# Kernel tuning notes

Measured on AMD Instinct MI355X. Metric: run time of the kernel, lower is better.

## Reference

```python
import jax, jax.numpy as jnp
import numpy as np

# module config (matches init_kwargs, single stream, groups=1)
N, I = 4, 64            # batch, input channels
CR, CA, CO = 64, 64, 64 # recurrent, attention, out channels
HEADS, S = 4, 3         # heads, spatial kernel
HC = CA // HEADS        # head channels = 16
H, W = 48, 48
INIT_I, INIT_F = -1.0, 1.0


def _conv(x, w, padding):
    # x: [N,C,H,W], w: [O,C,kh,kw]
    return jax.lax.conv_general_dilated(
        x, w, window_strides=(1, 1), padding=padding,
        dimension_numbers=('NCHW', 'OIHW', 'NCHW'))


def setup_inputs() -> dict:
    key = jax.random.key(0)
    ks = jax.random.split(key, 8)
    std = 0.05
    x = jax.random.normal(ks[0], (N, I, H, W), jnp.float32)
    W_in = jax.random.normal(ks[1], (CR, I), jnp.float32) * std      # 1x1 input conv
    b_in = jnp.zeros((CR,), jnp.float32)
    # 4 combos (xx, xh, hx, hh), each a 3x3 conv CR->CA, no bias
    Wq = jax.random.normal(ks[2], (4, CA, CR, S, S), jnp.float32) * std * (HC ** -0.5)
    Wk = jax.random.normal(ks[3], (4, CA, CR, S, S), jnp.float32) * std
    Wv = jax.random.normal(ks[4], (4, CA, CR, S, S), jnp.float32) * std
    # gate projections: 4 gates (i,f,g,o) x 4 attn branches, each 1x1 CA->CR
    Wproj = jax.random.normal(ks[5], (4, 4, CR, CA), jnp.float32) * std * 0.5
    b_gates = jnp.array([INIT_I, INIT_F, 0.0, 0.0], jnp.float32)[:, None] * jnp.ones((4, CR), jnp.float32)
    W_out = jax.random.normal(ks[6], (CO, CR), jnp.float32) * std    # 1x1 out conv
    b_out = jnp.zeros((CO,), jnp.float32)
    return {"x": x, "W_in": W_in, "b_in": b_in, "Wq": Wq, "Wk": Wk, "Wv": Wv,
            "Wproj": Wproj, "b_gates": b_gates, "W_out": W_out, "b_out": b_out}


def reference(x, W_in, b_in, Wq, Wk, Wv, Wproj, b_gates, W_out, b_out):
    n, _, hh, ww = x.shape
    # input projection (Accumulate of one 1x1 conv, bias 0)
    xin = jnp.einsum('nchw,oc->nohw', x, W_in) + b_in[None, :, None, None]
    h = jnp.zeros_like(xin)  # cold start: past is empty -> h = c = 0
    pairs = ((xin, xin), (xin, h), (h, xin), (h, h))
    attns = []
    for idx, (query, token) in enumerate(pairs):
        # q: SAME-padded 3x3 conv -> Q = H*W tokens; k/v: VALID -> D = (H-2)*(W-2)
        q = _conv(query, Wq[idx], 'SAME').reshape(n, HEADS, HC, -1)    # [n,h,c,Q]
        k = _conv(token, Wk[idx], 'VALID').reshape(n, HEADS, HC, -1)   # [n,h,c,D]
        v = _conv(token, Wv[idx], 'VALID').reshape(n, HEADS, HC, -1)   # [n,h,c,D]
        w = jax.nn.softmax(jnp.einsum('nhcq,nhcd->nhqd', q, k), axis=-1)
        a = jnp.einsum('nhcd,nhqd->nhcq', v, w).reshape(n, CA, hh, ww)
        attns.append(a)
    A = jnp.stack(attns, axis=0)  # [4, n, CA, H, W]
    # Accumulate of 4 1x1 projections per gate + gate bias
    pre = jnp.einsum('anchw,gaoc->gnohw', A, Wproj) + b_gates[:, None, :, None, None]
    i = jax.nn.sigmoid(pre[0])
    f = jax.nn.sigmoid(pre[1])
    g = jnp.tanh(pre[2])
    o = jax.nn.sigmoid(pre[3])
    c = i * g          # c_prev = 0, so f*c_prev vanishes
    hout = o * jnp.tanh(c)  # dropout p=0 -> identity
    return jnp.einsum('nchw,oc->nohw', hout, W_out) + b_out[None, :, None, None]
```

## Files before the change

### kernel.cpp

```cpp
#include <hip/hip_runtime.h>
#include <math.h>

#define NB   4
#define CIN  64
#define HH   48
#define WW   48
#define HW   2304
#define DH   46
#define DW   46
#define DD   2116
#define NHEAD 4
#define HC   16
#define NT   136
#define QTL  144

typedef short  s4 __attribute__((ext_vector_type(4)));
typedef short  s8 __attribute__((ext_vector_type(8)));
typedef float  f4 __attribute__((ext_vector_type(4)));

__global__ __launch_bounds__(256) void k_xin(const float* __restrict__ x,
                                             const float* __restrict__ Win,
                                             const float* __restrict__ bin,
                                             unsigned short* __restrict__ xb) {
    int cell = blockIdx.x * 256 + threadIdx.x;
    if (cell >= 2500) return;
    int n = blockIdx.y, ocg = blockIdx.z;
    int cy = cell / 50, cx = cell - cy * 50;
    float a[4] = {0.f, 0.f, 0.f, 0.f};
    if (cy >= 1 && cy <= 48 && cx >= 1 && cx <= 48) {
        int px = (cy - 1) * 48 + (cx - 1);
        const float* xp = x + (size_t)(n * CIN) * HW + px;
        #pragma unroll
        for (int j = 0; j < 4; ++j) a[j] = bin[ocg * 4 + j];
        #pragma unroll 8
        for (int ic = 0; ic < CIN; ++ic) {
            float xv = xp[ic * HW];
            a[0] += Win[(ocg * 4 + 0) * CIN + ic] * xv;
            a[1] += Win[(ocg * 4 + 1) * CIN + ic] * xv;
            a[2] += Win[(ocg * 4 + 2) * CIN + ic] * xv;
            a[3] += Win[(ocg * 4 + 3) * CIN + ic] * xv;
        }
    }
    s8 st;
    #pragma unroll
    for (int j = 0; j < 4; ++j) {
        unsigned u = __builtin_bit_cast(unsigned, a[j]);
        st[j] = (short)(u >> 16);
        float lo = a[j] - __builtin_bit_cast(float, u & 0xffff0000u);
        st[4 + j] = (short)(__builtin_bit_cast(unsigned, lo) >> 16);
    }
    *(s8*)(xb + ((size_t)(n * 2500 + cell)) * 128 + ocg * 8) = st;
}

__global__ __launch_bounds__(256) void k_wcvt(const float* __restrict__ Wq,
                                              const float* __restrict__ Wk,
                                              const float* __restrict__ Wv,
                                              unsigned short* __restrict__ Wb) {
    int bx = blockIdx.x;
    int cq = bx / 9, tap = bx - cq * 9;
    int cv = cq >> 2, ocq = cq & 3;
    const float* src = (cv == 0) ? Wq : (cv == 1) ? Wk : (cv == 2) ? Wv
                                                      : (Wv + 2 * CIN * CIN * 9);
    int t = threadIdx.x;
    int m = t >> 4, kl = t & 15, quad = kl >> 2, j = kl & 3;
    #pragma unroll
    for (int kq = 0; kq < 4; ++kq) {
        float v = src[((size_t)(ocq * 16 + m) * CIN + kq * 16 + kl) * 9 + tap];
        unsigned u = __builtin_bit_cast(unsigned, v);
        float lo = v - __builtin_bit_cast(float, u & 0xffff0000u);
        size_t base = ((size_t)(cq * 9 + tap) * 4 + kq) * 512 + m * 32 + quad * 8 + j;
        Wb[base]     = (unsigned short)(u >> 16);
        Wb[base + 4] = (unsigned short)(__builtin_bit_cast(unsigned, lo) >> 16);
    }
}

__global__ __launch_bounds__(256, 3) void k_conv(const unsigned short* __restrict__ xb,
                                                 const unsigned short* __restrict__ Wb,
                                                 float* __restrict__ q0, float* __restrict__ k0,
                                                 float* __restrict__ v0, float* __restrict__ v2) {
    int y = blockIdx.x, n = blockIdx.y, cv = blockIdx.z;
    float* ob; int outw, pd;
    if (cv == 0)      { ob = q0; outw = 48; pd = 0; }
    else if (cv == 1) { ob = k0; outw = 46; pd = 1; }
    else if (cv == 2) { ob = v0; outw = 46; pd = 1; }
    else              { ob = v2; outw = 46; pd = 1; }
    if (y >= outw) return;
    int lane = threadIdx.x & 63, wv = threadIdx.x >> 6;
    int m16 = lane & 15, quad = lane >> 4;
    const unsigned short* Wt = Wb + (size_t)(cv * 4 + wv) * 9 * 2048 + m16 * 32 + quad * 8;
    const unsigned short* B0 = xb + ((size_t)n * 2500 + (size_t)(y + pd) * 50 + pd + m16) * 128 + quad * 8;

    f4 a0 = {0.f, 0.f, 0.f, 0.f}, a1 = a0, a2 = a0;

    s8 w[4], c0[4], c1[4], c2[4];
    #pragma unroll
    for (int kq = 0; kq < 4; ++kq) {
        w[kq]  = *(const s8*)(Wt + kq * 512);
        c0[kq] = *(const s8*)(B0 + kq * 32);
        c1[kq] = *(const s8*)(B0 + 16 * 128 + kq * 32);
        c2[kq] = *(const s8*)(B0 + 32 * 128 + kq * 32);
    }

    #pragma unroll
    for (int tap = 0; tap < 9; ++tap) {
        s8 wn[4], n0[4], n1[4], n2[4];
        if (tap < 8) {
            int tn = tap + 1;
            int dy = tn / 3, dx = tn - dy * 3;
            const unsigned short* bp = B0 + (size_t)(dy * 50 + dx) * 128;
            const unsigned short* wp = Wt + tn * 2048;
            #pragma unroll
            for (int kq = 0; kq < 4; ++kq) {
                wn[kq] = *(const s8*)(wp + kq * 512);
                n0[kq] = *(const s8*)(bp + kq * 32);
                n1[kq] = *(const s8*)(bp + 16 * 128 + kq * 32);
                n2[kq] = *(const s8*)(bp + 32 * 128 + kq * 32);
            }
        }
        #pragma unroll
        for (int kq = 0; kq < 4; ++kq) {
            s4 ah  = __builtin_shufflevector(w[kq], w[kq], 0, 1, 2, 3);
            s4 al  = __builtin_shufflevector(w[kq], w[kq], 4, 5, 6, 7);
            s4 bh0 = __builtin_shufflevector(c0[kq], c0[kq], 0, 1, 2, 3);
            s4 bl0 = __builtin_shufflevector(c0[kq], c0[kq], 4, 5, 6, 7);
            s4 bh1 = __builtin_shufflevector(c1[kq], c1[kq], 0, 1, 2, 3);
            s4 bl1 = __builtin_shufflevector(c1[kq], c1[kq], 4, 5, 6, 7);
            s4 bh2 = __builtin_shufflevector(c2[kq], c2[kq], 0, 1, 2, 3);
            s4 bl2 = __builtin_shufflevector(c2[kq], c2[kq], 4, 5, 6, 7);
            a0 = __builtin_amdgcn_mfma_f32_16x16x16bf16_1k(ah, bh0, a0, 0, 0, 0);
            a1 = __builtin_amdgcn_mfma_f32_16x16x16bf16_1k(ah, bh1, a1, 0, 0, 0);
            a2 = __builtin_amdgcn_mfma_f32_16x16x16bf16_1k(ah, bh2, a2, 0, 0, 0);
            a0 = __builtin_amdgcn_mfma_f32_16x16x16bf16_1k(al, bh0, a0, 0, 0, 0);
            a1 = __builtin_amdgcn_mfma_f32_16x16x16bf16_1k(al, bh1, a1, 0, 0, 0);
            a2 = __builtin_amdgcn_mfma_f32_16x16x16bf16_1k(al, bh2, a2, 0, 0, 0);
            a0 = __builtin_amdgcn_mfma_f32_16x16x16bf16_1k(ah, bl0, a0, 0, 0, 0);
            a1 = __builtin_amdgcn_mfma_f32_16x16x16bf16_1k(ah, bl1, a1, 0, 0, 0);
            a2 = __builtin_amdgcn_mfma_f32_16x16x16bf16_1k(ah, bl2, a2, 0, 0, 0);
        }
        if (tap < 8) {
            #pragma unroll
            for (int kq = 0; kq < 4; ++kq) {
                w[kq] = wn[kq]; c0[kq] = n0[kq]; c1[kq] = n1[kq]; c2[kq] = n2[kq];
            }
        }
    }

    size_t outsz = (size_t)outw * outw;
    float* opb = ob + (size_t)(n * CIN + wv * 16 + quad * 4) * outsz + (size_t)y * outw;
    {
        float* op = opb + m16;
        op[0] = a0.x; op[outsz] = a0.y; op[2 * outsz] = a0.z; op[3 * outsz] = a0.w;
        op = opb + 16 + m16;
        op[0] = a1.x; op[outsz] = a1.y; op[2 * outsz] = a1.z; op[3 * outsz] = a1.w;
    }
    if (32 + m16 < outw) {
        float* op = opb + 32 + m16;
        op[0] = a2.x; op[outsz] = a2.y; op[2 * outsz] = a2.z; op[3 * outsz] = a2.w;
    }
}

__global__ __launch_bounds__(256) void k_cvt(const float* __restrict__ q0,
                                             const float* __restrict__ k0,
                                             const float* __restrict__ v0,
                                             unsigned short* __restrict__ Qb,
                                             unsigned short* __restrict__ Kb,
                                             unsigned short* __restrict__ Vb) {
    __shared__ float sm[272];
    int bx = blockIdx.x, nh = blockIdx.y;
    int n = nh >> 2, h = nh & 3;
    int t = threadIdx.x;
    {
        int c = t >> 4, q = t & 15;
        float val = q0[(size_t)(n * CIN + h * HC + c) * HW + bx * 16 + q];
        sm[c * 17 + q] = val;
        __syncthreads();
        int q2 = t >> 4, c2 = t & 15;
        float v = sm[c2 * 17 + q2];
        unsigned u = __builtin_bit_cast(unsigned, v);
        unsigned short* dst = Qb + (size_t)(nh * QTL + bx) * 512;
        dst[t] = (unsigned short)(u >> 16);
        float lo = v - __builtin_bit_cast(float, u & 0xffff0000u);
        dst[256 + t] = (unsigned short)(__builtin_bit_cast(unsigned, lo) >> 16);
    }
    if (bx < NT) {
        __syncthreads();
        int c = t >> 4, d = t & 15;
        int dgl = bx * 16 + d;
        float kv = (dgl < DD) ? k0[(size_t)(n * CIN + h * HC + c) * DD + dgl] : 0.f;
        sm[c * 17 + d] = kv;
        __syncthreads();
        {
            int d2 = t >> 4, c2 = t & 15;
            float v = sm[c2 * 17 + d2];
            unsigned u = __builtin_bit_cast(unsigned, v);
            unsigned short* dst = Kb + (size_t)(nh * NT + bx) * 512;
            dst[t] = (unsigned short)(u >> 16);
            float lo = v - __builtin_bit_cast(float, u & 0xffff0000u);
            dst[256 + t] = (unsigned short)(__builtin_bit_cast(unsigned, lo) >> 16);
        }
        {
            float vv = (dgl < DD) ? v0[(size_t)(n * CIN + h * HC + c) * DD + dgl] : 0.f;
            unsigned u = __builtin_bit_cast(unsigned, vv);
            unsigned short* dst = Vb + (size_t)(nh * NT + bx) * 512;
            dst[t] = (unsigned short)(u >> 16);
            float lo = vv - __builtin_bit_cast(float, u & 0xffff0000u);
            dst[256 + t] = (unsigned short)(__builtin_bit_cast(unsigned, lo) >> 16);
        }
    }
}

__global__ __launch_bounds__(256) void k_mattn(const unsigned short* __restrict__ Qb,
                                               const unsigned short* __restrict__ Kb,
                                               const unsigned short* __restrict__ Vb,
                                               float* __restrict__ part) {
    __shared__ float sO[4][4][256];
    __shared__ float sl[4][4][64];
    int strip = blockIdx.x >> 1, hb = blockIdx.x & 1, nh = blockIdx.y;
    int lane = threadIdx.x & 63, wv = threadIdx.x >> 6;
    int ds = hb * 4 + wv;
    int q16 = lane & 15, quad = lane >> 4;
    int foff = q16 * 16 + quad * 4;

    s4 qh[4], ql[4];
    #pragma unroll
    for (int j = 0; j < 4; ++j) {
        const unsigned short* Qp = Qb + (size_t)(nh * QTL + strip * 4 + j) * 512 + foff;
        qh[j] = *(const s4*)(Qp);
        ql[j] = *(const s4*)(Qp + 256);
    }
    f4 O[4];
    float l[4];
    #pragma unroll
    for (int j = 0; j < 4; ++j) { O[j] = (f4){0.f, 0.f, 0.f, 0.f}; l[j] = 0.f; }

    const unsigned short* Kp = Kb + (size_t)(nh * NT + ds * 17) * 512 + foff;
    const unsigned short* Vp = Vb + (size_t)(nh * NT + ds * 17) * 512 + foff;
    s4 khi = *(const s4*)(Kp);
    s4 klo = *(const s4*)(Kp + 256);
    s4 vhi = *(const s4*)(Vp);
    s4 vlo = *(const s4*)(Vp + 256);

    for (int it = 0; it < 17; ++it) {
        int nxt = (it < 16) ? (it + 1) * 512 : 0;
        s4 nkhi = *(const s4*)(Kp + nxt);
        s4 nklo = *(const s4*)(Kp + nxt + 256);
        s4 nvhi = *(const s4*)(Vp + nxt);
        s4 nvlo = *(const s4*)(Vp + nxt + 256);

        #pragma unroll
        for (int j = 0; j < 4; ++j) {
            f4 c1 = (f4){0.f, 0.f, 0.f, 0.f};
            c1 = __builtin_amdgcn_mfma_f32_16x16x16bf16_1k(khi, qh[j], c1, 0, 0, 0);
            c1 = __builtin_amdgcn_mfma_f32_16x16x16bf16_1k(klo, qh[j], c1, 0, 0, 0);
            c1 = __builtin_amdgcn_mfma_f32_16x16x16bf16_1k(khi, ql[j], c1, 0, 0, 0);
            float p0 = __expf(c1.x), p1 = __expf(c1.y);
            float p2 = __expf(c1.z), p3 = __expf(c1.w);
            l[j] += (p0 + p1) + (p2 + p3);
            unsigned u0 = __builtin_bit_cast(unsigned, p0);
            unsigned u1 = __builtin_bit_cast(unsigned, p1);
            unsigned u2 = __builtin_bit_cast(unsigned, p2);
            unsigned u3 = __builtin_bit_cast(unsigned, p3);
            s4 ph;
            ph.x = (short)(u0 >> 16); ph.y = (short)(u1 >> 16);
            ph.z = (short)(u2 >> 16); ph.w = (short)(u3 >> 16);
            float r0 = p0 - __builtin_bit_cast(float, u0 & 0xffff0000u);
            float r1 = p1 - __builtin_bit_cast(float, u1 & 0xffff0000u);
            float r2 = p2 - __builtin_bit_cast(float, u2 & 0xffff0000u);
            float r3 = p3 - __builtin_bit_cast(float, u3 & 0xffff0000u);
            s4 pl;
            pl.x = (short)(__builtin_bit_cast(unsigned, r0) >> 16);
            pl.y = (short)(__builtin_bit_cast(unsigned, r1) >> 16);
            pl.z = (short)(__builtin_bit_cast(unsigned, r2) >> 16);
            pl.w = (short)(__builtin_bit_cast(unsigned, r3) >> 16);
            O[j] = __builtin_amdgcn_mfma_f32_16x16x16bf16_1k(vhi, ph, O[j], 0, 0, 0);
            O[j] = __builtin_amdgcn_mfma_f32_16x16x16bf16_1k(vlo, ph, O[j], 0, 0, 0);
            O[j] = __builtin_amdgcn_mfma_f32_16x16x16bf16_1k(vhi, pl, O[j], 0, 0, 0);
        }
        khi = nkhi; klo = nklo; vhi = nvhi; vlo = nvlo;
    }

    #pragma unroll
    for (int j = 0; j < 4; ++j) {
        sO[wv][j][(quad * 4 + 0) * 16 + q16] = O[j].x;
        sO[wv][j][(quad * 4 + 1) * 16 + q16] = O[j].y;
        sO[wv][j][(quad * 4 + 2) * 16 + q16] = O[j].z;
        sO[wv][j][(quad * 4 + 3) * 16 + q16] = O[j].w;
        sl[wv][j][quad * 16 + q16] = l[j];
    }
    __syncthreads();
    int t = threadIdx.x;
    float* pb = part + (size_t)((nh * 36 + strip) * 2 + hb) * 1280;
    #pragma unroll
    for (int j = 0; j < 4; ++j)
        pb[j * 256 + t] = (sO[0][j][t] + sO[1][j][t]) + (sO[2][j][t] + sO[3][j][t]);
    {
        int j2 = t >> 6, i2 = t & 63;
        pb[1024 + t] = (sl[0][j2][i2] + sl[1][j2][i2]) + (sl[2][j2][i2] + sl[3][j2][i2]);
    }
}

__global__ __launch_bounds__(256) void k_acomb(const float* __restrict__ part,
                                               float* __restrict__ a0) {
    int strip = blockIdx.x, nh = blockIdx.y;
    int n = nh >> 2, h = nh & 3;
    const float* b0 = part + (size_t)((nh * 36 + strip) * 2) * 1280;
    const float* b1 = b0 + 1280;
    int t = threadIdx.x;
    int q = t & 15, c = t >> 4;
    #pragma unroll
    for (int j = 0; j < 4; ++j) {
        float lsum = 0.f;
        #pragma unroll
        for (int qd = 0; qd < 4; ++qd)
            lsum += b0[1024 + j * 64 + qd * 16 + q] + b1[1024 + j * 64 + qd * 16 + q];
        float inv = 1.f / (lsum - 60.f);
        float v = (b0[j * 256 + c * 16 + q] + b1[j * 256 + c * 16 + q]) * inv;
        a0[(size_t)(n * CIN + h * HC + c) * HW + strip * 64 + j * 16 + q] = v;
    }
}

__global__ __launch_bounds__(256) void k_mean(const float* __restrict__ v2,
                                              float* __restrict__ a2m) {
    int n = blockIdx.x >> 6, c = blockIdx.x & 63;
    const float* p = v2 + (size_t)(n * CIN + c) * DD;
    float s = 0.f;
    for (int d = threadIdx.x; d < DD; d += 256) s += p[d];
    #pragma unroll
    for (int off = 32; off > 0; off >>= 1) s += __shfl_down(s, off);
    __shared__ float red[4];
    int lane = threadIdx.x & 63, wv = threadIdx.x >> 6;
    if (lane == 0) red[wv] = s;
    __syncthreads();
    if (threadIdx.x == 0)
        a2m[blockIdx.x] = (red[0] + red[1] + red[2] + red[3]) * (1.f / 2116.f);
}

__global__ __launch_bounds__(256) void k_const2(const float* __restrict__ Wproj,
                                                const float* __restrict__ bg,
                                                const float* __restrict__ a2m,
                                                float* __restrict__ c2) {
    int n = blockIdx.x;
    int t = threadIdx.x;
    if (t >= 192) return;
    int gi = t >> 6, o = t & 63;
    int g = (gi == 0) ? 0 : (gi == 1) ? 2 : 3;
    float acc = bg[g * CIN + o];
    const float* wp = Wproj + ((size_t)(g * 4 + 2) * CIN + o) * CIN;
    for (int c = 0; c < CIN; ++c) acc += wp[c] * a2m[n * CIN + c];
    c2[(gi * NB + n) * CIN + o] = acc;
}

__global__ __launch_bounds__(256) void k_gates(const float* __restrict__ a0,
                                               const float* __restrict__ c2,
                                               const float* __restrict__ Wproj,
                                               const float* __restrict__ Wout,
                                               const float* __restrict__ bout,
                                               float* __restrict__ out) {
    __shared__ float a0s[64][16];
    __shared__ float wps[3][64][64];
    __shared__ float hs[16][68];
    int n = blockIdx.y;
    int p0 = blockIdx.x * 16;
    int tid = threadIdx.x;

    for (int idx = tid; idx < 1024; idx += 256) {
        int c = idx >> 4, px = idx & 15;
        a0s[c][px] = a0[(size_t)(n * CIN + c) * HW + p0 + px];
    }
    for (int idx = tid; idx < 12288; idx += 256) {
        int o = idx & 63; int rest = idx >> 6; int c = rest & 63; int gi = rest >> 6;
        int g = (gi == 0) ? 0 : (gi == 1) ? 2 : 3;
        wps[gi][c][o] = Wproj[((size_t)(g * 4 + 0) * CIN + o) * CIN + c];
    }
    __syncthreads();

    int o = tid & 63, pg = tid >> 6;
    float pi[4], pgt[4], po[4];
    {
        float ci = c2[(0 * NB + n) * CIN + o];
        float cg = c2[(1 * NB + n) * CIN + o];
        float co = c2[(2 * NB + n) * CIN + o];
        #pragma unroll
        for (int j = 0; j < 4; ++j) { pi[j] = ci; pgt[j] = cg; po[j] = co; }
    }
    const float4* a4 = (const float4*)&a0s[0][0];
    #pragma unroll 4
    for (int c = 0; c < 64; ++c) {
        float4 av = a4[c * 4 + pg];
        float w0 = wps[0][c][o], w1 = wps[1][c][o], w2 = wps[2][c][o];
        pi[0]  += w0 * av.x; pi[1]  += w0 * av.y; pi[2]  += w0 * av.z; pi[3]  += w0 * av.w;
        pgt[0] += w1 * av.x; pgt[1] += w1 * av.y; pgt[2] += w1 * av.z; pgt[3] += w1 * av.w;
        po[0]  += w2 * av.x; po[1]  += w2 * av.y; po[2]  += w2 * av.z; po[3]  += w2 * av.w;
    }
    #pragma unroll
    for (int j = 0; j < 4; ++j) {
        float ii = 1.f / (1.f + __expf(-pi[j]));
        float gg = tanhf(pgt[j]);
        float oo = 1.f / (1.f + __expf(-po[j]));
        float cc = ii * gg;
        hs[pg * 4 + j][o] = oo * tanhf(cc);
    }
    __syncthreads();
    float acc[4];
    float bo = bout[o];
    #pragma unroll
    for (int j = 0; j < 4; ++j) acc[j] = bo;
    const float* wo = Wout + o * CIN;
    #pragma unroll 2
    for (int cg_ = 0; cg_ < 16; ++cg_) {
        float w0 = wo[cg_ * 4 + 0], w1 = wo[cg_ * 4 + 1], w2 = wo[cg_ * 4 + 2], w3 = wo[cg_ * 4 + 3];
        #pragma unroll
        for (int j = 0; j < 4; ++j) {
            const float4 hv = *(const float4*)&hs[pg * 4 + j][cg_ * 4];
            acc[j] += w0 * hv.x + w1 * hv.y + w2 * hv.z + w3 * hv.w;
        }
    }
    #pragma unroll
    for (int j = 0; j < 4; ++j)
        out[(size_t)(n * CIN + o) * HW + p0 + pg * 4 + j] = acc[j];
}

extern "C" void kernel_launch(void* const* d_in, const int* in_sizes, int n_in,
                              void* d_out, int out_size, void* d_ws, size_t ws_size,
                              hipStream_t stream) {
    const float* x     = (const float*)d_in[0];
    const float* W_in  = (const float*)d_in[1];
    const float* b_in  = (const float*)d_in[2];
    const float* Wq    = (const float*)d_in[3];
    const float* Wk    = (const float*)d_in[4];
    const float* Wv    = (const float*)d_in[5];
    const float* Wproj = (const float*)d_in[6];
    const float* b_g   = (const float*)d_in[7];
    const float* W_out = (const float*)d_in[8];
    const float* b_out = (const float*)d_in[9];
    float* out = (float*)d_out;

    float* q0   = (float*)d_ws;
    float* k0   = q0 + 589824;
    float* v0   = k0 + 541696;
    float* v2   = v0 + 541696;
    float* a0   = v2 + 541696;
    float* a2m  = a0 + 589824;
    float* c2   = a2m + 256;
    float* part = c2 + 768;
    unsigned short* Qb = (unsigned short*)(part + 1474560);
    unsigned short* Kb = Qb + (size_t)16 * QTL * 512;
    unsigned short* Vb = Kb + (size_t)16 * NT * 512;
    unsigned short* xb = Vb + (size_t)16 * NT * 512;
    unsigned short* Wb = xb + (size_t)4 * 2500 * 128;

    k_xin   <<<dim3(10, 4, 16), 256, 0, stream>>>(x, W_in, b_in, xb);
    k_wcvt  <<<dim3(144), 256, 0, stream>>>(Wq, Wk, Wv, Wb);
    k_conv  <<<dim3(48, 4, 4), 256, 0, stream>>>(xb, Wb, q0, k0, v0, v2);
    k_cvt   <<<dim3(144, 16), 256, 0, stream>>>(q0, k0, v0, Qb, Kb, Vb);
    k_mattn <<<dim3(72, 16), 256, 0, stream>>>(Qb, Kb, Vb, part);
    k_acomb <<<dim3(36, 16), 256, 0, stream>>>(part, a0);
    k_mean  <<<dim3(256), 256, 0, stream>>>(v2, a2m);
    k_const2<<<dim3(4), 256, 0, stream>>>(Wproj, b_g, a2m, c2);
    k_gates <<<dim3(144, 4), 256, 0, stream>>>(a0, c2, Wproj, W_out, b_out, out);
}
```

Before: 206.9 us.

## Merge prep kernels, fold attention combine and gate constants into gates kernel

Combines the input-projection and weight-conversion kernels into one launch with block-index dispatch. Removes the k_acomb and k_const2 kernels by computing the softmax normalisation and branch-2 gate constants inside k_gates directly from the partial attention buffers. Also adds sched_group_barrier hints in the conv MFMA loop to interleave loads and MFMAs. This cuts launches and the a0 round trip through global memory, at the cost of redundant per-block constant computation in k_gates.

```diff
diff --git a/kernel.cpp b/kernel.cpp
--- a/kernel.cpp
+++ b/kernel.cpp
@@ -18,59 +18,61 @@
 typedef short  s8 __attribute__((ext_vector_type(8)));
 typedef float  f4 __attribute__((ext_vector_type(4)));
 
-__global__ __launch_bounds__(256) void k_xin(const float* __restrict__ x,
-                                             const float* __restrict__ Win,
-                                             const float* __restrict__ bin,
-                                             unsigned short* __restrict__ xb) {
-    int cell = blockIdx.x * 256 + threadIdx.x;
-    if (cell >= 2500) return;
-    int n = blockIdx.y, ocg = blockIdx.z;
-    int cy = cell / 50, cx = cell - cy * 50;
-    float a[4] = {0.f, 0.f, 0.f, 0.f};
-    if (cy >= 1 && cy <= 48 && cx >= 1 && cx <= 48) {
-        int px = (cy - 1) * 48 + (cx - 1);
-        const float* xp = x + (size_t)(n * CIN) * HW + px;
-        #pragma unroll
-        for (int j = 0; j < 4; ++j) a[j] = bin[ocg * 4 + j];
-        #pragma unroll 8
-        for (int ic = 0; ic < CIN; ++ic) {
-            float xv = xp[ic * HW];
-            a[0] += Win[(ocg * 4 + 0) * CIN + ic] * xv;
-            a[1] += Win[(ocg * 4 + 1) * CIN + ic] * xv;
-            a[2] += Win[(ocg * 4 + 2) * CIN + ic] * xv;
-            a[3] += Win[(ocg * 4 + 3) * CIN + ic] * xv;
-        }
-    }
-    s8 st;
-    #pragma unroll
-    for (int j = 0; j < 4; ++j) {
-        unsigned u = __builtin_bit_cast(unsigned, a[j]);
-        st[j] = (short)(u >> 16);
-        float lo = a[j] - __builtin_bit_cast(float, u & 0xffff0000u);
-        st[4 + j] = (short)(__builtin_bit_cast(unsigned, lo) >> 16);
-    }
-    *(s8*)(xb + ((size_t)(n * 2500 + cell)) * 128 + ocg * 8) = st;
-}
-
-__global__ __launch_bounds__(256) void k_wcvt(const float* __restrict__ Wq,
-                                              const float* __restrict__ Wk,
-                                              const float* __restrict__ Wv,
-                                              unsigned short* __restrict__ Wb) {
-    int bx = blockIdx.x;
-    int cq = bx / 9, tap = bx - cq * 9;
-    int cv = cq >> 2, ocq = cq & 3;
-    const float* src = (cv == 0) ? Wq : (cv == 1) ? Wk : (cv == 2) ? Wv
-                                                      : (Wv + 2 * CIN * CIN * 9);
-    int t = threadIdx.x;
-    int m = t >> 4, kl = t & 15, quad = kl >> 2, j = kl & 3;
-    #pragma unroll
-    for (int kq = 0; kq < 4; ++kq) {
-        float v = src[((size_t)(ocq * 16 + m) * CIN + kq * 16 + kl) * 9 + tap];
-        unsigned u = __builtin_bit_cast(unsigned, v);
-        float lo = v - __builtin_bit_cast(float, u & 0xffff0000u);
-        size_t base = ((size_t)(cq * 9 + tap) * 4 + kq) * 512 + m * 32 + quad * 8 + j;
-        Wb[base]     = (unsigned short)(u >> 16);
-        Wb[base + 4] = (unsigned short)(__builtin_bit_cast(unsigned, lo) >> 16);
+__global__ __launch_bounds__(256) void k_xw(const float* __restrict__ x,
+                                            const float* __restrict__ Win,
+                                            const float* __restrict__ bin,
+                                            const float* __restrict__ Wq,
+                                            const float* __restrict__ Wk,
+                                            const float* __restrict__ Wv,
+                                            unsigned short* __restrict__ xb,
+                                            unsigned short* __restrict__ Wb) {
+    int b = blockIdx.x;
+    if (b < 640) {
+        int bx = b % 10, n = (b / 10) & 3, ocg = b / 40;
+        int cell = bx * 256 + threadIdx.x;
+        if (cell >= 2500) return;
+        int cy = cell / 50, cx = cell - cy * 50;
+        float a[4] = {0.f, 0.f, 0.f, 0.f};
+        if (cy >= 1 && cy <= 48 && cx >= 1 && cx <= 48) {
+            int px = (cy - 1) * 48 + (cx - 1);
+            const float* xp = x + (size_t)(n * CIN) * HW + px;
+            #pragma unroll
+            for (int j = 0; j < 4; ++j) a[j] = bin[ocg * 4 + j];
+            #pragma unroll 8
+            for (int ic = 0; ic < CIN; ++ic) {
+                float xv = xp[ic * HW];
+                a[0] += Win[(ocg * 4 + 0) * CIN + ic] * xv;
+                a[1] += Win[(ocg * 4 + 1) * CIN + ic] * xv;
+                a[2] += Win[(ocg * 4 + 2) * CIN + ic] * xv;
+                a[3] += Win[(ocg * 4 + 3) * CIN + ic] * xv;
+            }
+        }
+        s8 st;
+        #pragma unroll
+        for (int j = 0; j < 4; ++j) {
+            unsigned u = __builtin_bit_cast(unsigned, a[j]);
+            st[j] = (short)(u >> 16);
+            float lo = a[j] - __builtin_bit_cast(float, u & 0xffff0000u);
+            st[4 + j] = (short)(__builtin_bit_cast(unsigned, lo) >> 16);
+        }
+        *(s8*)(xb + ((size_t)(n * 2500 + cell)) * 128 + ocg * 8) = st;
+    } else {
+        int bx = b - 640;
+        int cq = bx / 9, tap = bx - cq * 9;
+        int cv = cq >> 2, ocq = cq & 3;
+        const float* src = (cv == 0) ? Wq : (cv == 1) ? Wk : (cv == 2) ? Wv
+                                                          : (Wv + 2 * CIN * CIN * 9);
+        int t = threadIdx.x;
+        int m = t >> 4, kl = t & 15, quad = kl >> 2, j = kl & 3;
+        #pragma unroll
+        for (int kq = 0; kq < 4; ++kq) {
+            float v = src[((size_t)(ocq * 16 + m) * CIN + kq * 16 + kl) * 9 + tap];
+            unsigned u = __builtin_bit_cast(unsigned, v);
+            float lo = v - __builtin_bit_cast(float, u & 0xffff0000u);
+            size_t base = ((size_t)(cq * 9 + tap) * 4 + kq) * 512 + m * 32 + quad * 8 + j;
+            Wb[base]     = (unsigned short)(u >> 16);
+            Wb[base + 4] = (unsigned short)(__builtin_bit_cast(unsigned, lo) >> 16);
+        }
     }
 }
 
@@ -97,9 +99,10 @@
     for (int kq = 0; kq < 4; ++kq) {
         w[kq]  = *(const s8*)(Wt + kq * 512);
         c0[kq] = *(const s8*)(B0 + kq * 32);
-        c1[kq] = *(const s8*)(B0 + 16 * 128 + kq * 32);
-        c2[kq] = *(const s8*)(B0 + 32 * 128 + kq * 32);
-    }
+        c1[kq] = *(const s8*)(B0 + 2048 + kq * 32);
+        c2[kq] = *(const s8*)(B0 + 4096 + kq * 32);
+    }
+    __builtin_amdgcn_sched_group_barrier(0x020, 16, 0);
 
     #pragma unroll
     for (int tap = 0; tap < 9; ++tap) {
@@ -107,14 +110,14 @@
         if (tap < 8) {
             int tn = tap + 1;
             int dy = tn / 3, dx = tn - dy * 3;
-            const unsigned short* bp = B0 + (size_t)(dy * 50 + dx) * 128;
+            const unsigned short* bq = B0 + (size_t)(dy * 50 + dx) * 128;
             const unsigned short* wp = Wt + tn * 2048;
             #pragma unroll
             for (int kq = 0; kq < 4; ++kq) {
                 wn[kq] = *(const s8*)(wp + kq * 512);
-                n0[kq] = *(const s8*)(bp + kq * 32);
-                n1[kq] = *(const s8*)(bp + 16 * 128 + kq * 32);
-                n2[kq] = *(const s8*)(bp + 32 * 128 + kq * 32);
+                n0[kq] = *(const s8*)(bq + kq * 32);
+                n1[kq] = *(const s8*)(bq + 2048 + kq * 32);
+                n2[kq] = *(const s8*)(bq + 4096 + kq * 32);
             }
         }
         #pragma unroll
@@ -137,6 +140,8 @@
             a1 = __builtin_amdgcn_mfma_f32_16x16x16bf16_1k(ah, bl1, a1, 0, 0, 0);
             a2 = __builtin_amdgcn_mfma_f32_16x16x16bf16_1k(ah, bl2, a2, 0, 0, 0);
         }
+        if (tap < 8) __builtin_amdgcn_sched_group_barrier(0x020, 16, 0);
+        __builtin_amdgcn_sched_group_barrier(0x008, 36, 0);
         if (tap < 8) {
             #pragma unroll
             for (int kq = 0; kq < 4; ++kq) {
@@ -299,26 +304,6 @@
     }
 }
 
-__global__ __launch_bounds__(256) void k_acomb(const float* __restrict__ part,
-                                               float* __restrict__ a0) {
-    int strip = blockIdx.x, nh = blockIdx.y;
-    int n = nh >> 2, h = nh & 3;
-    const float* b0 = part + (size_t)((nh * 36 + strip) * 2) * 1280;
-    const float* b1 = b0 + 1280;
-    int t = threadIdx.x;
-    int q = t & 15, c = t >> 4;
-    #pragma unroll
-    for (int j = 0; j < 4; ++j) {
-        float lsum = 0.f;
-        #pragma unroll
-        for (int qd = 0; qd < 4; ++qd)
-            lsum += b0[1024 + j * 64 + qd * 16 + q] + b1[1024 + j * 64 + qd * 16 + q];
-        float inv = 1.f / (lsum - 60.f);
-        float v = (b0[j * 256 + c * 16 + q] + b1[j * 256 + c * 16 + q]) * inv;
-        a0[(size_t)(n * CIN + h * HC + c) * HW + strip * 64 + j * 16 + q] = v;
-    }
-}
-
 __global__ __launch_bounds__(256) void k_mean(const float* __restrict__ v2,
                                               float* __restrict__ a2m) {
     int n = blockIdx.x >> 6, c = blockIdx.x & 63;
@@ -335,37 +320,52 @@
         a2m[blockIdx.x] = (red[0] + red[1] + red[2] + red[3]) * (1.f / 2116.f);
 }
 
-__global__ __launch_bounds__(256) void k_const2(const float* __restrict__ Wproj,
-                                                const float* __restrict__ bg,
-                                                const float* __restrict__ a2m,
-                                                float* __restrict__ c2) {
-    int n = blockIdx.x;
-    int t = threadIdx.x;
-    if (t >= 192) return;
-    int gi = t >> 6, o = t & 63;
-    int g = (gi == 0) ? 0 : (gi == 1) ? 2 : 3;
-    float acc = bg[g * CIN + o];
-    const float* wp = Wproj + ((size_t)(g * 4 + 2) * CIN + o) * CIN;
-    for (int c = 0; c < CIN; ++c) acc += wp[c] * a2m[n * CIN + c];
-    c2[(gi * NB + n) * CIN + o] = acc;
-}
-
-__global__ __launch_bounds__(256) void k_gates(const float* __restrict__ a0,
-                                               const float* __restrict__ c2,
+__global__ __launch_bounds__(256) void k_gates(const float* __restrict__ part,
+                                               const float* __restrict__ a2m,
                                                const float* __restrict__ Wproj,
+                                               const float* __restrict__ bg,
                                                const float* __restrict__ Wout,
                                                const float* __restrict__ bout,
                                                float* __restrict__ out) {
     __shared__ float a0s[64][16];
     __shared__ float wps[3][64][64];
     __shared__ float hs[16][68];
+    __shared__ float invs[4][16];
+    __shared__ float c2s[3][64];
     int n = blockIdx.y;
-    int p0 = blockIdx.x * 16;
+    int pt = blockIdx.x;
+    int strip = pt >> 2, jq = pt & 3;
+    int p0 = pt * 16;
     int tid = threadIdx.x;
+
+    if (tid < 64) {
+        int h = tid >> 4, q = tid & 15;
+        const float* b0 = part + (size_t)(((n * 4 + h) * 36 + strip) * 2) * 1280;
+        const float* b1 = b0 + 1280;
+        float s = 0.f;
+        #pragma unroll
+        for (int quad = 0; quad < 4; ++quad)
+            s += b0[1024 + jq * 64 + quad * 16 + q] + b1[1024 + jq * 64 + quad * 16 + q];
+        invs[h][q] = 1.f / (s - 60.f);
+    } else {
+        int gi = (tid - 64) >> 6, o = tid & 63;
+        int g = (gi == 0) ? 0 : (gi == 1) ? 2 : 3;
+        float acc = bg[g * CIN + o];
+        const float* wp = Wproj + ((size_t)(g * 4 + 2) * CIN + o) * CIN;
+        const float* am = a2m + n * CIN;
+        #pragma unroll 8
+        for (int c = 0; c < CIN; ++c) acc += wp[c] * am[c];
+        c2s[gi][o] = acc;
+    }
+    __syncthreads();
 
     for (int idx = tid; idx < 1024; idx += 256) {
         int c = idx >> 4, px = idx & 15;
-        a0s[c][px] = a0[(size_t)(n * CIN + c) * HW + p0 + px];
+        int h = c >> 4, c16 = c & 15;
+        const float* b0 = part + (size_t)(((n * 4 + h) * 36 + strip) * 2) * 1280;
+        const float* b1 = b0 + 1280;
+        int off = jq * 256 + c16 * 16 + px;
+        a0s[c][px] = (b0[off] + b1[off]) * invs[h][px];
     }
     for (int idx = tid; idx < 12288; idx += 256) {
         int o = idx & 63; int rest = idx >> 6; int c = rest & 63; int gi = rest >> 6;
@@ -377,9 +377,7 @@
     int o = tid & 63, pg = tid >> 6;
     float pi[4], pgt[4], po[4];
     {
-        float ci = c2[(0 * NB + n) * CIN + o];
-        float cg = c2[(1 * NB + n) * CIN + o];
-        float co = c2[(2 * NB + n) * CIN + o];
+        float ci = c2s[0][o], cg = c2s[1][o], co = c2s[2][o];
         #pragma unroll
         for (int j = 0; j < 4; ++j) { pi[j] = ci; pgt[j] = cg; po[j] = co; }
     }
@@ -439,23 +437,18 @@
     float* k0   = q0 + 589824;
     float* v0   = k0 + 541696;
     float* v2   = v0 + 541696;
-    float* a0   = v2 + 541696;
-    float* a2m  = a0 + 589824;
-    float* c2   = a2m + 256;
-    float* part = c2 + 768;
+    float* a2m  = v2 + 541696;
+    float* part = a2m + 256;
     unsigned short* Qb = (unsigned short*)(part + 1474560);
     unsigned short* Kb = Qb + (size_t)16 * QTL * 512;
     unsigned short* Vb = Kb + (size_t)16 * NT * 512;
     unsigned short* xb = Vb + (size_t)16 * NT * 512;
     unsigned short* Wb = xb + (size_t)4 * 2500 * 128;
 
-    k_xin   <<<dim3(10, 4, 16), 256, 0, stream>>>(x, W_in, b_in, xb);
-    k_wcvt  <<<dim3(144), 256, 0, stream>>>(Wq, Wk, Wv, Wb);
+    k_xw    <<<dim3(784), 256, 0, stream>>>(x, W_in, b_in, Wq, Wk, Wv, xb, Wb);
     k_conv  <<<dim3(48, 4, 4), 256, 0, stream>>>(xb, Wb, q0, k0, v0, v2);
     k_cvt   <<<dim3(144, 16), 256, 0, stream>>>(q0, k0, v0, Qb, Kb, Vb);
     k_mattn <<<dim3(72, 16), 256, 0, stream>>>(Qb, Kb, Vb, part);
-    k_acomb <<<dim3(36, 16), 256, 0, stream>>>(part, a0);
     k_mean  <<<dim3(256), 256, 0, stream>>>(v2, a2m);
-    k_const2<<<dim3(4), 256, 0, stream>>>(Wproj, b_g, a2m, c2);
-    k_gates <<<dim3(144, 4), 256, 0, stream>>>(a0, c2, Wproj, W_out, b_out, out);
-}
+    k_gates <<<dim3(144, 4), 256, 0, stream>>>(part, a2m, Wproj, b_g, W_out, b_out, out);
+}
```

Measured after the change: 205.3 us. About the same (-0.8%).
